# Kernel optimization log

Measured on AMD Instinct MI355X. Metric: run time of the kernel, lower is better.

The kernel has to match this reference:

```python
import jax, jax.numpy as jnp
import numpy as np

# ---- configuration (from init_kwargs / image geometry) ----
NUM_CLASSES = 10          # digit classes 1..10 (scores has K+1 cols, col 0 = background)
R = 500000                # total digit proposals for the image
T = 2048                  # topk_per_image: fixed-size survivor set for jit-friendly NMS
SCORE_T = 0.05            # digit_score_thresh
NMS_T = 0.5               # nms_thresh
IMG_W, IMG_H = 1920.0, 1080.0
CLS_OFFSET = IMG_W + IMG_H + 1.0  # batched_nms coordinate-offset trick (per-class NMS)


def setup_inputs() -> dict:
    key = jax.random.key(0)
    k1, k2, k3, k4 = jax.random.split(key, 4)
    # realistic boxes: uniform centers over the image, sizes in [10, 100] px
    cxcy = jax.random.uniform(k1, (R, 2)) * jnp.array([IMG_W, IMG_H], dtype=jnp.float32)
    wh = 10.0 + 90.0 * jax.random.uniform(k2, (R, 2))
    boxes = jnp.concatenate([cxcy - 0.5 * wh, cxcy + 0.5 * wh], axis=1)  # [R,4] x1y1x2y2
    # class probabilities over K+1 classes (col 0 = background)
    scores = jax.nn.softmax(jax.random.normal(k3, (R, NUM_CLASSES + 1)), axis=1)
    # per-box digit-center score (pred_digit_center_scores)
    center_scores = jax.random.uniform(k4, (R,))
    return {"boxes": boxes, "scores": scores, "center_scores": center_scores}


def _iou_matrix(b):
    # b: [T,4] in x1y1x2y2. Returns [T,T] pairwise IoU.
    area = jnp.clip(b[:, 2] - b[:, 0], 0.0) * jnp.clip(b[:, 3] - b[:, 1], 0.0)  # [T]
    lt = jnp.maximum(b[:, None, :2], b[None, :, :2])  # [T,T,2]
    rb = jnp.minimum(b[:, None, 2:], b[None, :, 2:])  # [T,T,2]
    wh = jnp.clip(rb - lt, 0.0)
    inter = wh[..., 0] * wh[..., 1]
    return inter / (area[:, None] + area[None, :] - inter + 1e-9)


def reference(boxes, scores, center_scores):
    # 1) drop background column, fuse with digit-center scores
    fg = scores[:, 1:] * center_scores[:, None]            # [R,K]
    # 2) clip boxes to image (Boxes.clip)
    clipped = jnp.stack([
        jnp.clip(boxes[:, 0], 0.0, IMG_W),
        jnp.clip(boxes[:, 1], 0.0, IMG_H),
        jnp.clip(boxes[:, 2], 0.0, IMG_W),
        jnp.clip(boxes[:, 3], 0.0, IMG_H),
    ], axis=1)                                             # [R,4]
    # 3) flatten (box, class) candidates and threshold (filter_mask = scores > thresh)
    flat = fg.reshape(-1)                                  # [R*K]
    masked = jnp.where(flat > SCORE_T, flat, -1.0)
    # 4) fixed-size pre-filter: top-T candidates by fused score
    vals, idx = jax.lax.top_k(masked, T)                   # sorted descending
    cand_boxes = clipped[idx // NUM_CLASSES]               # [T,4]
    cand_cls = idx % NUM_CLASSES                           # [T] (cls_id - 1)
    valid = vals > SCORE_T
    # 5) per-class batched NMS via coordinate-offset trick
    nms_boxes = cand_boxes + cand_cls.astype(cand_boxes.dtype)[:, None] * CLS_OFFSET
    iou = _iou_matrix(nms_boxes)                           # [T,T]
    rng = jnp.arange(T)
    def body(i, keep):
        sup = keep[i] & (iou[i] > NMS_T) & (rng > i)
        return keep & jnp.logical_not(sup)
    keep = jax.lax.fori_loop(0, T, body, valid)            # greedy NMS (inputs sorted by score)
    # 6) masked fixed-shape outputs: kept boxes + kept scores
    out_boxes = jnp.where(keep[:, None], cand_boxes, 0.0)
    out_scores = jnp.where(keep, vals, 0.0)
    return jnp.concatenate([out_boxes, out_scores[:, None]], axis=1)  # [T,5]
```

## Files before the change

### kernel.cpp

```cpp
#include <hip/hip_runtime.h>
#include <stdint.h>

typedef unsigned int u32;
typedef unsigned long long u64;

#define SCORE_THR 0.05f
#define NMS_THR   0.5f
#define TK        2048
#define CAP       4096
#define BASE14    ((int)(0x3D4CCCCDu >> 14))
#define MAGIC11   3123612579ull
#define NREP      8
#define PAIR_CAP  16384
#define SGRID     256
#define SBLK      1024
#define RBLK      4

#define WS_OFFS   0
#define WS_BINPOS 16384
#define WS_HDR    32768
#define WS_CBX    33024
#define WS_NBX    65792
#define WS_VALS   98560
#define WS_HREP   106752
#define WS_BUF    237824
#define WS_PAIRS  269824

__global__ __launch_bounds__(SBLK) void k_hist(const float* __restrict__ scores,
                                               const float* __restrict__ center,
                                               int R, u32* __restrict__ hrep) {
    __shared__ u32 h[8192];
    for (int t = threadIdx.x; t < 8192; t += blockDim.x) h[t] = 0;
    __syncthreads();
    u32 rep = ((u32)threadIdx.x & 1u) << 12;
    int total_e = R * 11;
    int nq = total_e >> 2;
    int qpb = (nq + (int)gridDim.x - 1) / (int)gridDim.x;
    int start = (int)blockIdx.x * qpb;
    int end = start + qpb; if (end > nq) end = nq;
    int bd = (int)blockDim.x;
    for (int q = start + (int)threadIdx.x; q < end; q += 4 * bd) {
        int q1 = q + bd, q2 = q + 2 * bd, q3 = q + 3 * bd;
        float4 va, vb, vc, vd;
        bool ga = true, gb = q1 < end, gc = q2 < end, gd = q3 < end;
        va = ((const float4*)scores)[q];
        if (gb) vb = ((const float4*)scores)[q1];
        if (gc) vc = ((const float4*)scores)[q2];
        if (gd) vd = ((const float4*)scores)[q3];
#define HPROC(g, qq, v4)                                                   \
        if (g) {                                                           \
            float vv[4] = {v4.x, v4.y, v4.z, v4.w};                        \
            _Pragma("unroll")                                              \
            for (int j = 0; j < 4; j++) {                                  \
                u32 e2 = ((u32)(qq) << 2) + (u32)j;                        \
                u32 r = (u32)(((u64)e2 * MAGIC11) >> 35);                  \
                u32 c = e2 - r * 11u;                                      \
                if (c != 0u) {                                             \
                    float s = __fmul_rn(vv[j], center[r]);                 \
                    if (s > SCORE_THR) {                                   \
                        u32 key = __float_as_uint(s);                      \
                        int b = (int)(key >> 14) - BASE14;                 \
                        b = min(max(b, 0), 4095);                          \
                        atomicAdd(&h[rep | (u32)b], 1u);                   \
                    }                                                      \
                }                                                          \
            }                                                              \
        }
        HPROC(ga, q, va) HPROC(gb, q1, vb) HPROC(gc, q2, vc) HPROC(gd, q3, vd)
#undef HPROC
    }
    if (blockIdx.x == 0 && threadIdx.x == 0) {
        for (int e2 = nq << 2; e2 < total_e; e2++) {
            u32 r = (u32)(((u64)(u32)e2 * MAGIC11) >> 35);
            u32 c = (u32)e2 - r * 11u;
            if (c != 0u) {
                float s = __fmul_rn(scores[e2], center[r]);
                if (s > SCORE_THR) {
                    u32 key = __float_as_uint(s);
                    int b = (int)(key >> 14) - BASE14;
                    b = min(max(b, 0), 4095);
                    atomicAdd(&h[b], 1u);
                }
            }
        }
    }
    __syncthreads();
    u32* hout = hrep + (size_t)(blockIdx.x & (NREP - 1)) * 4096;
    for (int t = threadIdx.x; t < 4096; t += blockDim.x) {
        u32 s = h[t] + h[4096 + t];
        if (s) atomicAdd(&hout[t], s);
    }
}

__global__ void k_scan(const u32* __restrict__ hrep, u32* __restrict__ offs,
                       u32* __restrict__ binpos, u32* hdr,
                       float* __restrict__ cand_bx, float* __restrict__ nms_bx,
                       float* __restrict__ vals) {
    __shared__ u32 wsum[4];
    int t = threadIdx.x;
    u32 P = hdr[60];
    int base = 4096 - 16 * (t + 1);
    u32 v[16];
    u32 segsum = 0;
#pragma unroll
    for (int j = 0; j < 16; j++) {
        u32 s = 0;
#pragma unroll
        for (int i = 0; i < NREP; i++) s += hrep[i * 4096 + base + j];
        s -= 8u * P;
        v[j] = s; segsum += s;
    }
    u32 incl = segsum;
#pragma unroll
    for (int off = 1; off < 64; off <<= 1) {
        u32 x = (u32)__shfl_up((int)incl, off);
        if ((t & 63) >= off) incl += x;
    }
    if ((t & 63) == 63) wsum[t >> 6] = incl;
    __syncthreads();
    u32 woff = 0;
    for (int w = 0; w < (t >> 6); w++) woff += wsum[w];
    u32 total = wsum[0] + wsum[1] + wsum[2] + wsum[3];
    incl += woff;
    u32 excl = incl - segsum;
    u32 run = excl;
#pragma unroll
    for (int j = 15; j >= 0; j--) {
        offs[base + j] = run;
        binpos[base + j] = run;
        run += v[j];
    }
    if (t == 0) { hdr[6] = total; hdr[8] = 0; }
    if (total < (u32)TK) {
        if (t == 0) { hdr[3] = 0; hdr[5] = total; }
        for (int i = t; i < TK; i += 256) {
            ((float4*)cand_bx)[i] = make_float4(0.f, 0.f, 0.f, 0.f);
            ((float4*)nms_bx)[i]  = make_float4(0.f, 0.f, 0.f, 0.f);
            vals[i] = 0.f;
        }
        return;
    }
    if ((excl < (u32)TK) && (incl >= (u32)TK)) {
        u32 cum = excl;
#pragma unroll
        for (int j = 15; j >= 0; j--) {
            u32 nc = cum + v[j];
            if (nc >= (u32)TK) { hdr[3] = (u32)(base + j); hdr[5] = nc; break; }
            cum = nc;
        }
    }
}

__global__ __launch_bounds__(SBLK) void k_collect(const float* __restrict__ scores,
                                                  const float* __restrict__ center,
                                                  int R, const u32* __restrict__ hdr,
                                                  u32* __restrict__ binpos,
                                                  u64* __restrict__ buf) {
    u32 thr = hdr[3];
    int total_e = R * 11;
    int nq = total_e >> 2;
    int qpb = (nq + (int)gridDim.x - 1) / (int)gridDim.x;
    int start = (int)blockIdx.x * qpb;
    int end = start + qpb; if (end > nq) end = nq;
    int bd = (int)blockDim.x;
    for (int q = start + (int)threadIdx.x; q < end; q += 4 * bd) {
        int q1 = q + bd, q2 = q + 2 * bd, q3 = q + 3 * bd;
        float4 va, vb, vc, vd;
        bool ga = true, gb = q1 < end, gc = q2 < end, gd = q3 < end;
        va = ((const float4*)scores)[q];
        if (gb) vb = ((const float4*)scores)[q1];
        if (gc) vc = ((const float4*)scores)[q2];
        if (gd) vd = ((const float4*)scores)[q3];
#define CPROC(g, qq, v4)                                                   \
        if (g) {                                                           \
            float vv[4] = {v4.x, v4.y, v4.z, v4.w};                        \
            _Pragma("unroll")                                              \
            for (int j = 0; j < 4; j++) {                                  \
                u32 e2 = ((u32)(qq) << 2) + (u32)j;                        \
                u32 r = (u32)(((u64)e2 * MAGIC11) >> 35);                  \
                u32 c = e2 - r * 11u;                                      \
                if (c != 0u) {                                             \
                    float s = __fmul_rn(vv[j], center[r]);                 \
                    if (s > SCORE_THR) {                                   \
                        u32 key = __float_as_uint(s);                      \
                        int b = (int)(key >> 14) - BASE14;                 \
                        b = min(max(b, 0), 4095);                          \
                        if ((u32)b >= thr) {                               \
                            u32 pos = atomicAdd(&binpos[b], 1u);           \
                            if (pos < CAP) {                               \
                                u32 idx = r * 10u + (c - 1u);              \
                                buf[pos] = ((u64)key << 32) | (u64)(~idx); \
                            }                                              \
                        }                                                  \
                    }                                                      \
                }                                                          \
            }                                                              \
        }
        CPROC(ga, q, va) CPROC(gb, q1, vb) CPROC(gc, q2, vc) CPROC(gd, q3, vd)
#undef CPROC
    }
    if (blockIdx.x == 0 && threadIdx.x == 0) {
        for (int e2 = nq << 2; e2 < total_e; e2++) {
            u32 r = (u32)(((u64)(u32)e2 * MAGIC11) >> 35);
            u32 c = (u32)e2 - r * 11u;
            if (c != 0u) {
                float s = __fmul_rn(scores[e2], center[r]);
                if (s > SCORE_THR) {
                    u32 key = __float_as_uint(s);
                    int b = (int)(key >> 14) - BASE14;
                    b = min(max(b, 0), 4095);
                    if ((u32)b >= thr) {
                        u32 pos = atomicAdd(&binpos[b], 1u);
                        if (pos < CAP) {
                            u32 idx = r * 10u + (c - 1u);
                            buf[pos] = ((u64)key << 32) | (u64)(~idx);
                        }
                    }
                }
            }
        }
    }
}

__global__ __launch_bounds__(1024) void k_rank(
        const float* __restrict__ boxes, const u32* __restrict__ offs,
        const u32* __restrict__ hdr, const u64* __restrict__ buf,
        float* __restrict__ cand_bx, float* __restrict__ nms_bx,
        float* __restrict__ vals) {
    __shared__ u64 kb[CAP];
    __shared__ u32 lo[4096];
    int tid = threadIdx.x;
    u32 n = hdr[5]; if (n > (u32)CAP) n = CAP;
    u32 total = hdr[6];
    for (int t = tid; t < CAP; t += 1024) kb[t] = (t < (int)n) ? buf[t] : 0ull;
    for (int t = tid; t < 4096; t += 1024) lo[t] = offs[t];
    __syncthreads();
    int i = tid * RBLK + (int)blockIdx.x;
    if (i < (int)n) {
        u64 x = kb[i];
        u32 key = (u32)(x >> 32);
        int b = (int)(key >> 14) - BASE14;
        b = min(max(b, 0), 4095);
        u32 start = lo[b];
        u32 end = (b > 0) ? lo[b - 1] : total;
        if (end > (u32)CAP) end = CAP;
        u32 rk = start;
        for (u32 j = start; j < end; j++) rk += (kb[j] > x) ? 1u : 0u;
        if (rk < (u32)TK) {
            u32 idx = ~(u32)x;
            u32 r = idx / 10u, cls = idx % 10u;
            const float* bp = boxes + (size_t)r * 4;
            float c0 = fminf(fmaxf(bp[0], 0.f), 1920.f);
            float c1 = fminf(fmaxf(bp[1], 0.f), 1080.f);
            float c2 = fminf(fmaxf(bp[2], 0.f), 1920.f);
            float c3 = fminf(fmaxf(bp[3], 0.f), 1080.f);
            float offv = __fmul_rn((float)cls, 3001.0f);
            cand_bx[rk * 4 + 0] = c0; cand_bx[rk * 4 + 1] = c1;
            cand_bx[rk * 4 + 2] = c2; cand_bx[rk * 4 + 3] = c3;
            nms_bx[rk * 4 + 0] = __fadd_rn(c0, offv);
            nms_bx[rk * 4 + 1] = __fadd_rn(c1, offv);
            nms_bx[rk * 4 + 2] = __fadd_rn(c2, offv);
            nms_bx[rk * 4 + 3] = __fadd_rn(c3, offv);
            vals[rk] = __uint_as_float(key);
        }
    }
}

__global__ void k_mask(const float* __restrict__ nms_bx, u32* __restrict__ hdr,
                       u32* __restrict__ pairs) {
    int colbase = blockIdx.x * 64, rowbase = blockIdx.y * 64;
    if (colbase + 63 <= rowbase) return;
    __shared__ float4 cb[64];
    __shared__ float ca[64];
    int tid = threadIdx.x;
    float4 c = ((const float4*)nms_bx)[colbase + tid];
    cb[tid] = c;
    ca[tid] = __fmul_rn(fmaxf(__fsub_rn(c.z, c.x), 0.f),
                        fmaxf(__fsub_rn(c.w, c.y), 0.f));
    int row = rowbase + tid;
    float4 rb = ((const float4*)nms_bx)[row];
    float rarea = __fmul_rn(fmaxf(__fsub_rn(rb.z, rb.x), 0.f),
                            fmaxf(__fsub_rn(rb.w, rb.y), 0.f));
    __syncthreads();
    for (int cc = 0; cc < 64; cc++) {
        int col = colbase + cc;
        if (col > row) {
            float4 cbv = cb[cc];
            float ltx = fmaxf(rb.x, cbv.x), lty = fmaxf(rb.y, cbv.y);
            float rbx = fminf(rb.z, cbv.z), rby = fminf(rb.w, cbv.w);
            float w = fmaxf(__fsub_rn(rbx, ltx), 0.f);
            float h = fmaxf(__fsub_rn(rby, lty), 0.f);
            float inter = __fmul_rn(w, h);
            float denom = __fadd_rn(__fsub_rn(__fadd_rn(rarea, ca[cc]), inter), 1e-9f);
            float iou = __fdiv_rn(inter, denom);
            if (iou > NMS_THR) {
                u32 p = atomicAdd(&hdr[8], 1u);
                if (p < PAIR_CAP)
                    pairs[p] = ((u32)row << 11) | (u32)col;
            }
        }
    }
}

__global__ __launch_bounds__(64) void k_final(
        const u32* __restrict__ pairs, const u32* __restrict__ hdr,
        const float* __restrict__ vals, const float* __restrict__ cand_bx,
        float* __restrict__ out) {
    __shared__ u32 sp[PAIR_CAP];
    __shared__ u32 cur[2048];
    int lane = threadIdx.x;
    u32 np = hdr[8]; if (np > (u32)PAIR_CAP) np = PAIR_CAP;
    const float4* vp = (const float4*)vals + (size_t)lane * 8;
    float4 vv[8];
#pragma unroll
    for (int j = 0; j < 8; j++) vv[j] = vp[j];
    u32 validw = 0;
#pragma unroll
    for (int j = 0; j < 8; j++) {
        validw |= (vv[j].x > SCORE_THR ? 1u : 0u) << (4 * j + 0);
        validw |= (vv[j].y > SCORE_THR ? 1u : 0u) << (4 * j + 1);
        validw |= (vv[j].z > SCORE_THR ? 1u : 0u) << (4 * j + 2);
        validw |= (vv[j].w > SCORE_THR ? 1u : 0u) << (4 * j + 3);
    }
    for (int t = lane; t < 2048; t += 64) cur[t] = 0;
    __syncthreads();
    for (u32 k = lane; k < np; k += 64) atomicAdd(&cur[pairs[k] >> 11], 1u);
    __syncthreads();
    u32 cnt[32];
    u32 seg = 0;
#pragma unroll
    for (int j = 0; j < 32; j++) { cnt[j] = cur[lane * 32 + j]; seg += cnt[j]; }
    u32 incl = seg;
    for (int off = 1; off < 64; off <<= 1) {
        u32 t = (u32)__shfl_up((int)incl, off);
        if (lane >= off) incl += t;
    }
    u32 run = incl - seg;
#pragma unroll
    for (int j = 0; j < 32; j++) { cur[lane * 32 + j] = run; run += cnt[j]; }
    __syncthreads();
    for (u32 k = lane; k < np; k += 64) {
        u32 p = pairs[k];
        u32 pos = atomicAdd(&cur[p >> 11], 1u);
        sp[pos] = p;
    }
    __syncthreads();
    u32 removed = 0;
    for (u32 k = 0; k < np; k++) {
        u32 p = sp[k];
        u32 row = p >> 11, col = p & 2047u;
        u32 aw = (u32)__shfl((int)(validw & ~removed), (int)(row >> 5));
        if ((aw >> (row & 31)) & 1u)
            if (lane == (int)(col >> 5)) removed |= 1u << (col & 31);
    }
    u32 keepw = validw & ~removed;
#pragma unroll
    for (int b = 0; b < 32; b++) {
        int i = lane * 32 + b;
        bool kp = (keepw >> b) & 1u;
        const float4 bx = ((const float4*)cand_bx)[i];
        float v = (b & 3) == 0 ? vv[b >> 2].x :
                  (b & 3) == 1 ? vv[b >> 2].y :
                  (b & 3) == 2 ? vv[b >> 2].z : vv[b >> 2].w;
        out[i * 5 + 0] = kp ? bx.x : 0.f;
        out[i * 5 + 1] = kp ? bx.y : 0.f;
        out[i * 5 + 2] = kp ? bx.z : 0.f;
        out[i * 5 + 3] = kp ? bx.w : 0.f;
        out[i * 5 + 4] = kp ? v : 0.f;
    }
}

extern "C" void kernel_launch(void* const* d_in, const int* in_sizes, int n_in,
                              void* d_out, int out_size, void* d_ws, size_t ws_size,
                              hipStream_t stream) {
    const float* boxes = (const float*)d_in[0];
    const float* scores = (const float*)d_in[1];
    const float* center = (const float*)d_in[2];
    float* out = (float*)d_out;
    int R = in_sizes[2];

    char* w = (char*)d_ws;
    u32* offs   = (u32*)(w + WS_OFFS);
    u32* binpos = (u32*)(w + WS_BINPOS);
    u32* hdr    = (u32*)(w + WS_HDR);
    float* cbx  = (float*)(w + WS_CBX);
    float* nbx  = (float*)(w + WS_NBX);
    float* vls  = (float*)(w + WS_VALS);
    u32* hrep   = (u32*)(w + WS_HREP);
    u64* buf    = (u64*)(w + WS_BUF);
    u32* pairs  = (u32*)(w + WS_PAIRS);

    k_hist<<<SGRID, SBLK, 0, stream>>>(scores, center, R, hrep);
    k_scan<<<1, 256, 0, stream>>>(hrep, offs, binpos, hdr, cbx, nbx, vls);
    k_collect<<<SGRID, SBLK, 0, stream>>>(scores, center, R, hdr, binpos, buf);
    k_rank<<<RBLK, 1024, 0, stream>>>(boxes, offs, hdr, buf, cbx, nbx, vls);
    k_mask<<<dim3(32, 32), 64, 0, stream>>>(nbx, hdr, pairs);
    k_final<<<1, 64, 0, stream>>>(pairs, hdr, vls, cbx, out);
}
```

Before: 121.0 us.

## Fuse six pipeline kernels into one cooperative kernel with grid syncs

```diff
diff --git a/kernel.cpp b/kernel.cpp
--- a/kernel.cpp
+++ b/kernel.cpp
@@ -1,5 +1,8 @@
 #include <hip/hip_runtime.h>
+#include <hip/hip_cooperative_groups.h>
 #include <stdint.h>
+
+namespace cg = cooperative_groups;
 
 typedef unsigned int u32;
 typedef unsigned long long u64;
@@ -12,8 +15,8 @@
 #define MAGIC11   3123612579ull
 #define NREP      8
 #define PAIR_CAP  16384
-#define SGRID     256
-#define SBLK      1024
+#define GRID      256
+#define BLK       1024
 #define RBLK      4
 
 #define WS_OFFS   0
@@ -26,347 +29,356 @@
 #define WS_BUF    237824
 #define WS_PAIRS  269824
 
-__global__ __launch_bounds__(SBLK) void k_hist(const float* __restrict__ scores,
-                                               const float* __restrict__ center,
-                                               int R, u32* __restrict__ hrep) {
-    __shared__ u32 h[8192];
-    for (int t = threadIdx.x; t < 8192; t += blockDim.x) h[t] = 0;
-    __syncthreads();
-    u32 rep = ((u32)threadIdx.x & 1u) << 12;
-    int total_e = R * 11;
-    int nq = total_e >> 2;
-    int qpb = (nq + (int)gridDim.x - 1) / (int)gridDim.x;
-    int start = (int)blockIdx.x * qpb;
-    int end = start + qpb; if (end > nq) end = nq;
-    int bd = (int)blockDim.x;
-    for (int q = start + (int)threadIdx.x; q < end; q += 4 * bd) {
-        int q1 = q + bd, q2 = q + 2 * bd, q3 = q + 3 * bd;
-        float4 va, vb, vc, vd;
-        bool ga = true, gb = q1 < end, gc = q2 < end, gd = q3 < end;
-        va = ((const float4*)scores)[q];
-        if (gb) vb = ((const float4*)scores)[q1];
-        if (gc) vc = ((const float4*)scores)[q2];
-        if (gd) vd = ((const float4*)scores)[q3];
+__global__ __launch_bounds__(BLK, 1) void k_all(
+        const float* __restrict__ boxes, const float* __restrict__ scores,
+        const float* __restrict__ center, int R,
+        u32* offs, u32* binpos, u32* hdr,
+        float* cand_bx, float* nms_bx, float* vals,
+        u32* hrep, u64* buf, u32* pairs, float* out) {
+    __shared__ __align__(16) char smem[73728];
+    __shared__ u32 swsum[4];
+    cg::grid_group gg = cg::this_grid();
+    const u32 P = hdr[60];
+    const int tid = (int)threadIdx.x;
+    const int bid = (int)blockIdx.x;
+    const int total_e = R * 11;
+    const int nq = total_e >> 2;
+
+    {
+        u32* h = (u32*)smem;
+        for (int t = tid; t < 8192; t += BLK) h[t] = 0;
+        __syncthreads();
+        u32 rep = ((u32)tid & 1u) << 12;
+        int qpb = (nq + GRID - 1) / GRID;
+        int start = bid * qpb;
+        int end = start + qpb; if (end > nq) end = nq;
+        for (int q = start + tid; q < end; q += 4 * BLK) {
+            int q1 = q + BLK, q2 = q + 2 * BLK, q3 = q + 3 * BLK;
+            float4 va, vb, vc, vd;
+            bool ga = true, gb = q1 < end, gc = q2 < end, gd = q3 < end;
+            va = ((const float4*)scores)[q];
+            if (gb) vb = ((const float4*)scores)[q1];
+            if (gc) vc = ((const float4*)scores)[q2];
+            if (gd) vd = ((const float4*)scores)[q3];
 #define HPROC(g, qq, v4)                                                   \
-        if (g) {                                                           \
-            float vv[4] = {v4.x, v4.y, v4.z, v4.w};                        \
-            _Pragma("unroll")                                              \
-            for (int j = 0; j < 4; j++) {                                  \
-                u32 e2 = ((u32)(qq) << 2) + (u32)j;                        \
-                u32 r = (u32)(((u64)e2 * MAGIC11) >> 35);                  \
-                u32 c = e2 - r * 11u;                                      \
-                if (c != 0u) {                                             \
-                    float s = __fmul_rn(vv[j], center[r]);                 \
-                    if (s > SCORE_THR) {                                   \
-                        u32 key = __float_as_uint(s);                      \
-                        int b = (int)(key >> 14) - BASE14;                 \
-                        b = min(max(b, 0), 4095);                          \
-                        atomicAdd(&h[rep | (u32)b], 1u);                   \
+            if (g) {                                                       \
+                float vv[4] = {v4.x, v4.y, v4.z, v4.w};                    \
+                _Pragma("unroll")                                          \
+                for (int j = 0; j < 4; j++) {                              \
+                    u32 e2 = ((u32)(qq) << 2) + (u32)j;                    \
+                    u32 r = (u32)(((u64)e2 * MAGIC11) >> 35);              \
+                    u32 c = e2 - r * 11u;                                  \
+                    if (c != 0u) {                                         \
+                        float s = __fmul_rn(vv[j], center[r]);             \
+                        if (s > SCORE_THR) {                               \
+                            u32 key = __float_as_uint(s);                  \
+                            int b = (int)(key >> 14) - BASE14;             \
+                            b = min(max(b, 0), 4095);                      \
+                            atomicAdd(&h[rep | (u32)b], 1u);               \
+                        }                                                  \
                     }                                                      \
                 }                                                          \
-            }                                                              \
-        }
-        HPROC(ga, q, va) HPROC(gb, q1, vb) HPROC(gc, q2, vc) HPROC(gd, q3, vd)
+            }
+            HPROC(ga, q, va) HPROC(gb, q1, vb) HPROC(gc, q2, vc) HPROC(gd, q3, vd)
 #undef HPROC
-    }
-    if (blockIdx.x == 0 && threadIdx.x == 0) {
-        for (int e2 = nq << 2; e2 < total_e; e2++) {
-            u32 r = (u32)(((u64)(u32)e2 * MAGIC11) >> 35);
-            u32 c = (u32)e2 - r * 11u;
-            if (c != 0u) {
-                float s = __fmul_rn(scores[e2], center[r]);
-                if (s > SCORE_THR) {
-                    u32 key = __float_as_uint(s);
-                    int b = (int)(key >> 14) - BASE14;
-                    b = min(max(b, 0), 4095);
-                    atomicAdd(&h[b], 1u);
+        }
+        if (bid == 0 && tid == 0) {
+            for (int e2 = nq << 2; e2 < total_e; e2++) {
+                u32 r = (u32)(((u64)(u32)e2 * MAGIC11) >> 35);
+                u32 c = (u32)e2 - r * 11u;
+                if (c != 0u) {
+                    float s = __fmul_rn(scores[e2], center[r]);
+                    if (s > SCORE_THR) {
+                        u32 key = __float_as_uint(s);
+                        int b = (int)(key >> 14) - BASE14;
+                        b = min(max(b, 0), 4095);
+                        atomicAdd(&h[b], 1u);
+                    }
                 }
             }
         }
-    }
-    __syncthreads();
-    u32* hout = hrep + (size_t)(blockIdx.x & (NREP - 1)) * 4096;
-    for (int t = threadIdx.x; t < 4096; t += blockDim.x) {
-        u32 s = h[t] + h[4096 + t];
-        if (s) atomicAdd(&hout[t], s);
-    }
-}
-
-__global__ void k_scan(const u32* __restrict__ hrep, u32* __restrict__ offs,
-                       u32* __restrict__ binpos, u32* hdr,
-                       float* __restrict__ cand_bx, float* __restrict__ nms_bx,
-                       float* __restrict__ vals) {
-    __shared__ u32 wsum[4];
-    int t = threadIdx.x;
-    u32 P = hdr[60];
-    int base = 4096 - 16 * (t + 1);
-    u32 v[16];
-    u32 segsum = 0;
-#pragma unroll
-    for (int j = 0; j < 16; j++) {
-        u32 s = 0;
-#pragma unroll
-        for (int i = 0; i < NREP; i++) s += hrep[i * 4096 + base + j];
-        s -= 8u * P;
-        v[j] = s; segsum += s;
-    }
-    u32 incl = segsum;
-#pragma unroll
-    for (int off = 1; off < 64; off <<= 1) {
-        u32 x = (u32)__shfl_up((int)incl, off);
-        if ((t & 63) >= off) incl += x;
-    }
-    if ((t & 63) == 63) wsum[t >> 6] = incl;
-    __syncthreads();
-    u32 woff = 0;
-    for (int w = 0; w < (t >> 6); w++) woff += wsum[w];
-    u32 total = wsum[0] + wsum[1] + wsum[2] + wsum[3];
-    incl += woff;
-    u32 excl = incl - segsum;
-    u32 run = excl;
-#pragma unroll
-    for (int j = 15; j >= 0; j--) {
-        offs[base + j] = run;
-        binpos[base + j] = run;
-        run += v[j];
-    }
-    if (t == 0) { hdr[6] = total; hdr[8] = 0; }
-    if (total < (u32)TK) {
-        if (t == 0) { hdr[3] = 0; hdr[5] = total; }
-        for (int i = t; i < TK; i += 256) {
-            ((float4*)cand_bx)[i] = make_float4(0.f, 0.f, 0.f, 0.f);
-            ((float4*)nms_bx)[i]  = make_float4(0.f, 0.f, 0.f, 0.f);
-            vals[i] = 0.f;
-        }
-        return;
-    }
-    if ((excl < (u32)TK) && (incl >= (u32)TK)) {
-        u32 cum = excl;
-#pragma unroll
-        for (int j = 15; j >= 0; j--) {
-            u32 nc = cum + v[j];
-            if (nc >= (u32)TK) { hdr[3] = (u32)(base + j); hdr[5] = nc; break; }
-            cum = nc;
-        }
-    }
-}
-
-__global__ __launch_bounds__(SBLK) void k_collect(const float* __restrict__ scores,
-                                                  const float* __restrict__ center,
-                                                  int R, const u32* __restrict__ hdr,
-                                                  u32* __restrict__ binpos,
-                                                  u64* __restrict__ buf) {
-    u32 thr = hdr[3];
-    int total_e = R * 11;
-    int nq = total_e >> 2;
-    int qpb = (nq + (int)gridDim.x - 1) / (int)gridDim.x;
-    int start = (int)blockIdx.x * qpb;
-    int end = start + qpb; if (end > nq) end = nq;
-    int bd = (int)blockDim.x;
-    for (int q = start + (int)threadIdx.x; q < end; q += 4 * bd) {
-        int q1 = q + bd, q2 = q + 2 * bd, q3 = q + 3 * bd;
-        float4 va, vb, vc, vd;
-        bool ga = true, gb = q1 < end, gc = q2 < end, gd = q3 < end;
-        va = ((const float4*)scores)[q];
-        if (gb) vb = ((const float4*)scores)[q1];
-        if (gc) vc = ((const float4*)scores)[q2];
-        if (gd) vd = ((const float4*)scores)[q3];
+        __syncthreads();
+        u32* hout = hrep + (size_t)(bid & (NREP - 1)) * 4096;
+        for (int t = tid; t < 4096; t += BLK) {
+            u32 s = h[t] + h[4096 + t];
+            if (s) atomicAdd(&hout[t], s);
+        }
+    }
+    gg.sync();
+
+    if (bid == 0) {
+        int t = tid;
+        int base = 4096 - 16 * (t + 1);
+        u32 v[16]; u32 segsum = 0; u32 incl = 0;
+        if (t < 256) {
+#pragma unroll
+            for (int j = 0; j < 16; j++) {
+                u32 s = 0;
+#pragma unroll
+                for (int i = 0; i < NREP; i++) s += hrep[i * 4096 + base + j];
+                s -= 8u * P;
+                v[j] = s; segsum += s;
+            }
+            incl = segsum;
+#pragma unroll
+            for (int off = 1; off < 64; off <<= 1) {
+                u32 x = (u32)__shfl_up((int)incl, off);
+                if ((t & 63) >= off) incl += x;
+            }
+            if ((t & 63) == 63) swsum[t >> 6] = incl;
+        }
+        __syncthreads();
+        u32 total = swsum[0] + swsum[1] + swsum[2] + swsum[3];
+        if (t < 256) {
+            u32 woff = 0;
+            for (int w = 0; w < (t >> 6); w++) woff += swsum[w];
+            incl += woff;
+            u32 excl = incl - segsum;
+            u32 run = excl;
+#pragma unroll
+            for (int j = 15; j >= 0; j--) {
+                offs[base + j] = run;
+                binpos[base + j] = run;
+                run += v[j];
+            }
+            if (t == 0) hdr[6] = total;
+            if (total >= (u32)TK && excl < (u32)TK && incl >= (u32)TK) {
+                u32 cum = excl;
+#pragma unroll
+                for (int j = 15; j >= 0; j--) {
+                    u32 nc = cum + v[j];
+                    if (nc >= (u32)TK) { hdr[3] = (u32)(base + j); hdr[5] = nc; break; }
+                    cum = nc;
+                }
+            }
+        }
+        if (total < (u32)TK) {
+            if (t == 0) { hdr[3] = 0; hdr[5] = total; }
+            for (int i = tid; i < TK; i += BLK) {
+                ((float4*)cand_bx)[i] = make_float4(0.f, 0.f, 0.f, 0.f);
+                ((float4*)nms_bx)[i]  = make_float4(0.f, 0.f, 0.f, 0.f);
+                vals[i] = 0.f;
+            }
+        }
+    }
+    gg.sync();
+
+    {
+        u32 thr = hdr[3];
+        int qpb = (nq + GRID - 1) / GRID;
+        int start = bid * qpb;
+        int end = start + qpb; if (end > nq) end = nq;
+        for (int q = start + tid; q < end; q += 4 * BLK) {
+            int q1 = q + BLK, q2 = q + 2 * BLK, q3 = q + 3 * BLK;
+            float4 va, vb, vc, vd;
+            bool ga = true, gb = q1 < end, gc = q2 < end, gd = q3 < end;
+            va = ((const float4*)scores)[q];
+            if (gb) vb = ((const float4*)scores)[q1];
+            if (gc) vc = ((const float4*)scores)[q2];
+            if (gd) vd = ((const float4*)scores)[q3];
 #define CPROC(g, qq, v4)                                                   \
-        if (g) {                                                           \
-            float vv[4] = {v4.x, v4.y, v4.z, v4.w};                        \
-            _Pragma("unroll")                                              \
-            for (int j = 0; j < 4; j++) {                                  \
-                u32 e2 = ((u32)(qq) << 2) + (u32)j;                        \
-                u32 r = (u32)(((u64)e2 * MAGIC11) >> 35);                  \
-                u32 c = e2 - r * 11u;                                      \
-                if (c != 0u) {                                             \
-                    float s = __fmul_rn(vv[j], center[r]);                 \
-                    if (s > SCORE_THR) {                                   \
-                        u32 key = __float_as_uint(s);                      \
-                        int b = (int)(key >> 14) - BASE14;                 \
-                        b = min(max(b, 0), 4095);                          \
-                        if ((u32)b >= thr) {                               \
-                            u32 pos = atomicAdd(&binpos[b], 1u);           \
-                            if (pos < CAP) {                               \
-                                u32 idx = r * 10u + (c - 1u);              \
-                                buf[pos] = ((u64)key << 32) | (u64)(~idx); \
+            if (g) {                                                       \
+                float vv[4] = {v4.x, v4.y, v4.z, v4.w};                    \
+                _Pragma("unroll")                                          \
+                for (int j = 0; j < 4; j++) {                              \
+                    u32 e2 = ((u32)(qq) << 2) + (u32)j;                    \
+                    u32 r = (u32)(((u64)e2 * MAGIC11) >> 35);              \
+                    u32 c = e2 - r * 11u;                                  \
+                    if (c != 0u) {                                         \
+                        float s = __fmul_rn(vv[j], center[r]);             \
+                        if (s > SCORE_THR) {                               \
+                            u32 key = __float_as_uint(s);                  \
+                            int b = (int)(key >> 14) - BASE14;             \
+                            b = min(max(b, 0), 4095);                      \
+                            if ((u32)b >= thr) {                           \
+                                u32 pos = atomicAdd(&binpos[b], 1u);       \
+                                if (pos < CAP) {                           \
+                                    u32 idx = r * 10u + (c - 1u);          \
+                                    buf[pos] = ((u64)key << 32) | (u64)(~idx); \
+                                }                                          \
                             }                                              \
                         }                                                  \
                     }                                                      \
                 }                                                          \
-            }                                                              \
-        }
-        CPROC(ga, q, va) CPROC(gb, q1, vb) CPROC(gc, q2, vc) CPROC(gd, q3, vd)
+            }
+            CPROC(ga, q, va) CPROC(gb, q1, vb) CPROC(gc, q2, vc) CPROC(gd, q3, vd)
 #undef CPROC
-    }
-    if (blockIdx.x == 0 && threadIdx.x == 0) {
-        for (int e2 = nq << 2; e2 < total_e; e2++) {
-            u32 r = (u32)(((u64)(u32)e2 * MAGIC11) >> 35);
-            u32 c = (u32)e2 - r * 11u;
-            if (c != 0u) {
-                float s = __fmul_rn(scores[e2], center[r]);
-                if (s > SCORE_THR) {
-                    u32 key = __float_as_uint(s);
-                    int b = (int)(key >> 14) - BASE14;
-                    b = min(max(b, 0), 4095);
-                    if ((u32)b >= thr) {
-                        u32 pos = atomicAdd(&binpos[b], 1u);
-                        if (pos < CAP) {
-                            u32 idx = r * 10u + (c - 1u);
-                            buf[pos] = ((u64)key << 32) | (u64)(~idx);
+        }
+        if (bid == 0 && tid == 0) {
+            for (int e2 = nq << 2; e2 < total_e; e2++) {
+                u32 r = (u32)(((u64)(u32)e2 * MAGIC11) >> 35);
+                u32 c = (u32)e2 - r * 11u;
+                if (c != 0u) {
+                    float s = __fmul_rn(scores[e2], center[r]);
+                    if (s > SCORE_THR) {
+                        u32 key = __float_as_uint(s);
+                        int b = (int)(key >> 14) - BASE14;
+                        b = min(max(b, 0), 4095);
+                        if ((u32)b >= thr) {
+                            u32 pos = atomicAdd(&binpos[b], 1u);
+                            if (pos < CAP) {
+                                u32 idx = r * 10u + (c - 1u);
+                                buf[pos] = ((u64)key << 32) | (u64)(~idx);
+                            }
                         }
                     }
                 }
             }
         }
     }
-}
-
-__global__ __launch_bounds__(1024) void k_rank(
-        const float* __restrict__ boxes, const u32* __restrict__ offs,
-        const u32* __restrict__ hdr, const u64* __restrict__ buf,
-        float* __restrict__ cand_bx, float* __restrict__ nms_bx,
-        float* __restrict__ vals) {
-    __shared__ u64 kb[CAP];
-    __shared__ u32 lo[4096];
-    int tid = threadIdx.x;
-    u32 n = hdr[5]; if (n > (u32)CAP) n = CAP;
-    u32 total = hdr[6];
-    for (int t = tid; t < CAP; t += 1024) kb[t] = (t < (int)n) ? buf[t] : 0ull;
-    for (int t = tid; t < 4096; t += 1024) lo[t] = offs[t];
-    __syncthreads();
-    int i = tid * RBLK + (int)blockIdx.x;
-    if (i < (int)n) {
-        u64 x = kb[i];
-        u32 key = (u32)(x >> 32);
-        int b = (int)(key >> 14) - BASE14;
-        b = min(max(b, 0), 4095);
-        u32 start = lo[b];
-        u32 end = (b > 0) ? lo[b - 1] : total;
-        if (end > (u32)CAP) end = CAP;
-        u32 rk = start;
-        for (u32 j = start; j < end; j++) rk += (kb[j] > x) ? 1u : 0u;
-        if (rk < (u32)TK) {
-            u32 idx = ~(u32)x;
-            u32 r = idx / 10u, cls = idx % 10u;
-            const float* bp = boxes + (size_t)r * 4;
-            float c0 = fminf(fmaxf(bp[0], 0.f), 1920.f);
-            float c1 = fminf(fmaxf(bp[1], 0.f), 1080.f);
-            float c2 = fminf(fmaxf(bp[2], 0.f), 1920.f);
-            float c3 = fminf(fmaxf(bp[3], 0.f), 1080.f);
-            float offv = __fmul_rn((float)cls, 3001.0f);
-            cand_bx[rk * 4 + 0] = c0; cand_bx[rk * 4 + 1] = c1;
-            cand_bx[rk * 4 + 2] = c2; cand_bx[rk * 4 + 3] = c3;
-            nms_bx[rk * 4 + 0] = __fadd_rn(c0, offv);
-            nms_bx[rk * 4 + 1] = __fadd_rn(c1, offv);
-            nms_bx[rk * 4 + 2] = __fadd_rn(c2, offv);
-            nms_bx[rk * 4 + 3] = __fadd_rn(c3, offv);
-            vals[rk] = __uint_as_float(key);
-        }
-    }
-}
-
-__global__ void k_mask(const float* __restrict__ nms_bx, u32* __restrict__ hdr,
-                       u32* __restrict__ pairs) {
-    int colbase = blockIdx.x * 64, rowbase = blockIdx.y * 64;
-    if (colbase + 63 <= rowbase) return;
-    __shared__ float4 cb[64];
-    __shared__ float ca[64];
-    int tid = threadIdx.x;
-    float4 c = ((const float4*)nms_bx)[colbase + tid];
-    cb[tid] = c;
-    ca[tid] = __fmul_rn(fmaxf(__fsub_rn(c.z, c.x), 0.f),
-                        fmaxf(__fsub_rn(c.w, c.y), 0.f));
-    int row = rowbase + tid;
-    float4 rb = ((const float4*)nms_bx)[row];
-    float rarea = __fmul_rn(fmaxf(__fsub_rn(rb.z, rb.x), 0.f),
-                            fmaxf(__fsub_rn(rb.w, rb.y), 0.f));
-    __syncthreads();
-    for (int cc = 0; cc < 64; cc++) {
-        int col = colbase + cc;
-        if (col > row) {
-            float4 cbv = cb[cc];
-            float ltx = fmaxf(rb.x, cbv.x), lty = fmaxf(rb.y, cbv.y);
-            float rbx = fminf(rb.z, cbv.z), rby = fminf(rb.w, cbv.w);
-            float w = fmaxf(__fsub_rn(rbx, ltx), 0.f);
-            float h = fmaxf(__fsub_rn(rby, lty), 0.f);
-            float inter = __fmul_rn(w, h);
-            float denom = __fadd_rn(__fsub_rn(__fadd_rn(rarea, ca[cc]), inter), 1e-9f);
-            float iou = __fdiv_rn(inter, denom);
-            if (iou > NMS_THR) {
-                u32 p = atomicAdd(&hdr[8], 1u);
-                if (p < PAIR_CAP)
-                    pairs[p] = ((u32)row << 11) | (u32)col;
-            }
-        }
-    }
-}
-
-__global__ __launch_bounds__(64) void k_final(
-        const u32* __restrict__ pairs, const u32* __restrict__ hdr,
-        const float* __restrict__ vals, const float* __restrict__ cand_bx,
-        float* __restrict__ out) {
-    __shared__ u32 sp[PAIR_CAP];
-    __shared__ u32 cur[2048];
-    int lane = threadIdx.x;
-    u32 np = hdr[8]; if (np > (u32)PAIR_CAP) np = PAIR_CAP;
-    const float4* vp = (const float4*)vals + (size_t)lane * 8;
-    float4 vv[8];
-#pragma unroll
-    for (int j = 0; j < 8; j++) vv[j] = vp[j];
-    u32 validw = 0;
-#pragma unroll
-    for (int j = 0; j < 8; j++) {
-        validw |= (vv[j].x > SCORE_THR ? 1u : 0u) << (4 * j + 0);
-        validw |= (vv[j].y > SCORE_THR ? 1u : 0u) << (4 * j + 1);
-        validw |= (vv[j].z > SCORE_THR ? 1u : 0u) << (4 * j + 2);
-        validw |= (vv[j].w > SCORE_THR ? 1u : 0u) << (4 * j + 3);
-    }
-    for (int t = lane; t < 2048; t += 64) cur[t] = 0;
-    __syncthreads();
-    for (u32 k = lane; k < np; k += 64) atomicAdd(&cur[pairs[k] >> 11], 1u);
-    __syncthreads();
-    u32 cnt[32];
-    u32 seg = 0;
-#pragma unroll
-    for (int j = 0; j < 32; j++) { cnt[j] = cur[lane * 32 + j]; seg += cnt[j]; }
-    u32 incl = seg;
-    for (int off = 1; off < 64; off <<= 1) {
-        u32 t = (u32)__shfl_up((int)incl, off);
-        if (lane >= off) incl += t;
-    }
-    u32 run = incl - seg;
-#pragma unroll
-    for (int j = 0; j < 32; j++) { cur[lane * 32 + j] = run; run += cnt[j]; }
-    __syncthreads();
-    for (u32 k = lane; k < np; k += 64) {
-        u32 p = pairs[k];
-        u32 pos = atomicAdd(&cur[p >> 11], 1u);
-        sp[pos] = p;
-    }
-    __syncthreads();
-    u32 removed = 0;
-    for (u32 k = 0; k < np; k++) {
-        u32 p = sp[k];
-        u32 row = p >> 11, col = p & 2047u;
-        u32 aw = (u32)__shfl((int)(validw & ~removed), (int)(row >> 5));
-        if ((aw >> (row & 31)) & 1u)
-            if (lane == (int)(col >> 5)) removed |= 1u << (col & 31);
-    }
-    u32 keepw = validw & ~removed;
-#pragma unroll
-    for (int b = 0; b < 32; b++) {
-        int i = lane * 32 + b;
-        bool kp = (keepw >> b) & 1u;
-        const float4 bx = ((const float4*)cand_bx)[i];
-        float v = (b & 3) == 0 ? vv[b >> 2].x :
-                  (b & 3) == 1 ? vv[b >> 2].y :
-                  (b & 3) == 2 ? vv[b >> 2].z : vv[b >> 2].w;
-        out[i * 5 + 0] = kp ? bx.x : 0.f;
-        out[i * 5 + 1] = kp ? bx.y : 0.f;
-        out[i * 5 + 2] = kp ? bx.z : 0.f;
-        out[i * 5 + 3] = kp ? bx.w : 0.f;
-        out[i * 5 + 4] = kp ? v : 0.f;
+    gg.sync();
+
+    if (bid < RBLK) {
+        u64* kb = (u64*)smem;
+        u32* lo = (u32*)(smem + 32768);
+        u32 n = hdr[5]; if (n > (u32)CAP) n = CAP;
+        u32 total = hdr[6];
+        for (int t = tid; t < CAP; t += BLK) kb[t] = (t < (int)n) ? buf[t] : 0ull;
+        for (int t = tid; t < 4096; t += BLK) lo[t] = offs[t];
+        __syncthreads();
+        int i = tid * RBLK + bid;
+        if (i < (int)n) {
+            u64 x = kb[i];
+            u32 key = (u32)(x >> 32);
+            int b = (int)(key >> 14) - BASE14;
+            b = min(max(b, 0), 4095);
+            u32 bs = lo[b];
+            u32 be = (b > 0) ? lo[b - 1] : total;
+            if (be > (u32)CAP) be = CAP;
+            u32 rk = bs;
+            for (u32 j = bs; j < be; j++) rk += (kb[j] > x) ? 1u : 0u;
+            if (rk < (u32)TK) {
+                u32 idx = ~(u32)x;
+                u32 r = idx / 10u, cls = idx % 10u;
+                const float* bp = boxes + (size_t)r * 4;
+                float c0 = fminf(fmaxf(bp[0], 0.f), 1920.f);
+                float c1 = fminf(fmaxf(bp[1], 0.f), 1080.f);
+                float c2 = fminf(fmaxf(bp[2], 0.f), 1920.f);
+                float c3 = fminf(fmaxf(bp[3], 0.f), 1080.f);
+                float offv = __fmul_rn((float)cls, 3001.0f);
+                cand_bx[rk * 4 + 0] = c0; cand_bx[rk * 4 + 1] = c1;
+                cand_bx[rk * 4 + 2] = c2; cand_bx[rk * 4 + 3] = c3;
+                nms_bx[rk * 4 + 0] = __fadd_rn(c0, offv);
+                nms_bx[rk * 4 + 1] = __fadd_rn(c1, offv);
+                nms_bx[rk * 4 + 2] = __fadd_rn(c2, offv);
+                nms_bx[rk * 4 + 3] = __fadd_rn(c3, offv);
+                vals[rk] = __uint_as_float(key);
+            }
+        }
+    }
+    gg.sync();
+
+    {
+        int w = tid >> 6, lane = tid & 63;
+        float4* cbw = (float4*)smem + w * 64;
+        float*  caw = (float*)(smem + 16384) + w * 64;
+        int t1d = bid * 16 + w;
+        int bx = t1d & 31, by = (t1d >> 5) & 31;
+        int colbase = bx * 64, rowbase = by * 64;
+        bool live = (t1d < 1024) && (colbase + 63 > rowbase);
+        float4 rb; float rarea = 0.f;
+        if (live) {
+            float4 c = ((const float4*)nms_bx)[colbase + lane];
+            cbw[lane] = c;
+            caw[lane] = __fmul_rn(fmaxf(__fsub_rn(c.z, c.x), 0.f),
+                                  fmaxf(__fsub_rn(c.w, c.y), 0.f));
+            rb = ((const float4*)nms_bx)[rowbase + lane];
+            rarea = __fmul_rn(fmaxf(__fsub_rn(rb.z, rb.x), 0.f),
+                              fmaxf(__fsub_rn(rb.w, rb.y), 0.f));
+        }
+        __syncthreads();
+        if (live) {
+            int row = rowbase + lane;
+            for (int cc = 0; cc < 64; cc++) {
+                int col = colbase + cc;
+                if (col > row) {
+                    float4 cbv = cbw[cc];
+                    float ltx = fmaxf(rb.x, cbv.x), lty = fmaxf(rb.y, cbv.y);
+                    float rbx = fminf(rb.z, cbv.z), rby = fminf(rb.w, cbv.w);
+                    float ww = fmaxf(__fsub_rn(rbx, ltx), 0.f);
+                    float hh = fmaxf(__fsub_rn(rby, lty), 0.f);
+                    float inter = __fmul_rn(ww, hh);
+                    float denom = __fadd_rn(__fsub_rn(__fadd_rn(rarea, caw[cc]),
+                                                      inter), 1e-9f);
+                    float iou = __fdiv_rn(inter, denom);
+                    if (iou > NMS_THR) {
+                        u32 praw = atomicAdd(&hdr[8], 1u) - P;
+                        if (praw < PAIR_CAP)
+                            pairs[praw] = ((u32)row << 11) | (u32)col;
+                    }
+                }
+            }
+        }
+    }
+    gg.sync();
+
+    if (bid == 0) {
+        u32* sp  = (u32*)smem;
+        u32* cur = (u32*)(smem + 65536);
+        int lane = tid & 63;
+        bool w0 = (tid < 64);
+        u32 np = hdr[8] - P; if (np > (u32)PAIR_CAP) np = PAIR_CAP;
+        u32 validw = 0;
+        if (w0) {
+            const float4* vp = (const float4*)vals + (size_t)lane * 8;
+#pragma unroll
+            for (int j = 0; j < 8; j++) {
+                float4 v4 = vp[j];
+                validw |= (v4.x > SCORE_THR ? 1u : 0u) << (4 * j + 0);
+                validw |= (v4.y > SCORE_THR ? 1u : 0u) << (4 * j + 1);
+                validw |= (v4.z > SCORE_THR ? 1u : 0u) << (4 * j + 2);
+                validw |= (v4.w > SCORE_THR ? 1u : 0u) << (4 * j + 3);
+            }
+        }
+        for (int t = tid; t < 2048; t += BLK) cur[t] = 0;
+        __syncthreads();
+        for (u32 k = (u32)tid; k < np; k += BLK)
+            atomicAdd(&cur[pairs[k] >> 11], 1u);
+        __syncthreads();
+        if (w0) {
+            u32 seg = 0;
+            for (int j = 0; j < 32; j++) seg += cur[lane * 32 + j];
+            u32 incl = seg;
+            for (int off = 1; off < 64; off <<= 1) {
+                u32 x = (u32)__shfl_up((int)incl, off);
+                if (lane >= off) incl += x;
+            }
+            u32 run = incl - seg;
+            for (int j = 0; j < 32; j++) {
+                u32 cj = cur[lane * 32 + j];
+                cur[lane * 32 + j] = run; run += cj;
+            }
+        }
+        __syncthreads();
+        for (u32 k = (u32)tid; k < np; k += BLK) {
+            u32 p = pairs[k];
+            u32 pos = atomicAdd(&cur[p >> 11], 1u);
+            if (pos < (u32)PAIR_CAP) sp[pos] = p;
+        }
+        __syncthreads();
+        if (w0) {
+            u32 removed = 0;
+            for (u32 k = 0; k < np; k++) {
+                u32 p = sp[k];
+                u32 row = p >> 11, col = p & 2047u;
+                u32 aw = (u32)__shfl((int)(validw & ~removed), (int)(row >> 5));
+                if ((aw >> (row & 31)) & 1u)
+                    if (lane == (int)(col >> 5)) removed |= 1u << (col & 31);
+            }
+            u32 keepw = validw & ~removed;
+#pragma unroll
+            for (int b = 0; b < 32; b++) {
+                int i = lane * 32 + b;
+                bool kp = (keepw >> b) & 1u;
+                const float4 bx = ((const float4*)cand_bx)[i];
+                float v = vals[i];
+                out[i * 5 + 0] = kp ? bx.x : 0.f;
+                out[i * 5 + 1] = kp ? bx.y : 0.f;
+                out[i * 5 + 2] = kp ? bx.z : 0.f;
+                out[i * 5 + 3] = kp ? bx.w : 0.f;
+                out[i * 5 + 4] = kp ? v : 0.f;
+            }
+        }
     }
 }
 
@@ -390,10 +402,10 @@
     u64* buf    = (u64*)(w + WS_BUF);
     u32* pairs  = (u32*)(w + WS_PAIRS);
 
-    k_hist<<<SGRID, SBLK, 0, stream>>>(scores, center, R, hrep);
-    k_scan<<<1, 256, 0, stream>>>(hrep, offs, binpos, hdr, cbx, nbx, vls);
-    k_collect<<<SGRID, SBLK, 0, stream>>>(scores, center, R, hdr, binpos, buf);
-    k_rank<<<RBLK, 1024, 0, stream>>>(boxes, offs, hdr, buf, cbx, nbx, vls);
-    k_mask<<<dim3(32, 32), 64, 0, stream>>>(nbx, hdr, pairs);
-    k_final<<<1, 64, 0, stream>>>(pairs, hdr, vls, cbx, out);
+    void* args[] = { (void*)&boxes, (void*)&scores, (void*)&center, (void*)&R,
+                     (void*)&offs, (void*)&binpos, (void*)&hdr,
+                     (void*)&cbx, (void*)&nbx, (void*)&vls,
+                     (void*)&hrep, (void*)&buf, (void*)&pairs, (void*)&out };
+    hipLaunchCooperativeKernel((void*)k_all, dim3(GRID), dim3(BLK),
+                               args, 0, stream);
 }
```

After: 261.7 us. 2.16x slower.
